# Optimization experiments

Measured on AMD Instinct MI355X. Metric: run time of the kernel, lower is better.

## Reference

```python
import jax, jax.numpy as jnp
import numpy as np

L = 4        # number of GCN layers
B = 1024     # batch of brain graphs
R = 116      # ROIs (AAL atlas)
EPS = 1e-5   # BatchNorm eps


def setup_inputs() -> dict:
    key = jax.random.key(0)
    ks = jax.random.split(key, 20)
    def rn(k, shape, scale=0.1):
        return jax.random.normal(k, shape, dtype=jnp.float32) * scale
    return {
        "X": jax.random.normal(ks[0], (B, R, 3), dtype=jnp.float32),
        "Z": jax.random.normal(ks[1], (B, R, R), dtype=jnp.float32),
        "aw1": rn(ks[2], (L, 3, 3)), "ab1": rn(ks[3], (L, 3)),
        "aw2": rn(ks[4], (L, R, R)), "ab2": rn(ks[5], (L, R)),
        "nw": rn(ks[6], (L, 3, 3)), "nb": rn(ks[7], (L, 3)),
        "ew": rn(ks[8], (L, R, R)), "eb": rn(ks[9], (L, R)),
        "gn_g": jnp.ones((L, R), jnp.float32), "gn_b": jnp.zeros((L, R), jnp.float32),
        "ge_g": jnp.ones((L, R), jnp.float32), "ge_b": jnp.zeros((L, R), jnp.float32),
        "dn_w": rn(ks[10], (L + 1, 3)), "dn_b": rn(ks[11], (L + 1,)),
        "dn_g": jnp.ones((L + 1,), jnp.float32), "dn_beta": jnp.zeros((L + 1,), jnp.float32),
        "de_w": rn(ks[12], (L + 1, 78)), "de_b": rn(ks[13], (L + 1,)),
        "de_g": jnp.ones((L + 1,), jnp.float32), "de_beta": jnp.zeros((L + 1,), jnp.float32),
        "cw1": rn(ks[14], (1024, R * 4 * (L + 1)), 0.02), "cb1": jnp.zeros((1024,), jnp.float32),
        "cw2": rn(ks[15], (2, 1024), 0.02), "cb2": jnp.zeros((2,), jnp.float32),
    }


def _bn3(x, g, b):
    # BatchNorm1d(C) in training mode on (N, C, L): stats over (N, L) per channel
    m = x.mean(axis=(0, 2), keepdims=True)
    v = x.var(axis=(0, 2), keepdims=True)
    return (x - m) * jax.lax.rsqrt(v + EPS) * g[None, :, None] + b[None, :, None]


def _down_node(X, w, b, g, beta):
    # ConvDownSample(3): Conv1d(1,1,3) on (B*R,1,3) -> scalar per row, ReLU, BatchNorm1d(1)
    f = jax.nn.relu(X.reshape(-1, 3) @ w + b)                 # (B*R,)
    h = (f - f.mean()) * jax.lax.rsqrt(f.var() + EPS) * g + beta
    return h.reshape(X.shape[0], -1)                          # (B, R)


def _down_edge(Z, w, b, g, beta):
    # ConvDownSample(116): Conv1d(1,1,78,stride=39,pad=39) -> 3 outputs per row
    x = Z.reshape(-1, R)
    xp = jnp.pad(x, ((0, 0), (39, 39)))                       # (B*R, 194)
    win = jnp.stack([xp[:, 39 * t: 39 * t + 78] for t in range(3)], axis=1)  # (B*R,3,78)
    f = jax.nn.relu(win @ w + b)                              # (B*R, 3)
    h = (f - f.mean()) * jax.lax.rsqrt(f.var() + EPS) * g + beta
    return h.reshape(Z.shape[0], -1)                          # (B, 3R)


def reference(X, Z, aw1, ab1, aw2, ab2, nw, nb, ew, eb, gn_g, gn_b, ge_g, ge_b,
              dn_w, dn_b, dn_g, dn_beta, de_w, de_b, de_g, de_beta,
              cw1, cb1, cw2, cb2):
    xx = [_down_node(X, dn_w[0], dn_b[0], dn_g[0], dn_beta[0])]
    zz = [_down_edge(Z, de_w[0], de_b[0], de_g[0], de_beta[0])]
    for i in range(L):
        # Attention: K = conv1(X^T) (1x1 conv == matmul), Q = K^T, scores = Q@K
        K = jnp.einsum('oc,bnc->bon', aw1[i], X) + ab1[i][None, :, None]   # (B,3,R)
        att = jax.nn.softmax(jnp.einsum('bcn,bcm->bnm', K, K), axis=-1)    # (B,R,R)
        V = jnp.einsum('oc,bmc->bom', aw2[i], Z) + ab2[i][None, :, None]   # (B,R,R)
        A = jnp.einsum('bnk,bkm->bmn', att, V)                             # bmm + permute
        # Edge update
        Z1 = jnp.einsum('bnm,bmc->bnc', A, Z) @ ew[i].T + eb[i]
        Z = jax.nn.relu(_bn3(Z1, ge_g[i], ge_b[i])) + Z
        zz.append(_down_edge(Z, de_w[i + 1], de_b[i + 1], de_g[i + 1], de_beta[i + 1]))
        # Node update
        X1 = jnp.einsum('bnm,bmc->bnc', A, X) @ nw[i].T + nb[i]
        X = jax.nn.relu(_bn3(X1, gn_g[i], gn_b[i])) + X
        xx.append(_down_node(X, dn_w[i + 1], dn_b[i + 1], dn_g[i + 1], dn_beta[i + 1]))
    XZ = jnp.concatenate(xx + zz, axis=1)                     # (B, 116*4*(L+1))
    h = jax.nn.relu(XZ @ cw1.T + cb1)                         # dropout is identity (eval)
    return h @ cw2.T + cb2                                    # (B, 2)
```

## Files before the change

### kernel.cpp

```cpp
#include <hip/hip_runtime.h>
#if __has_include(<hip/hip_bf16.h>)
#include <hip/hip_bf16.h>
#define HAVE_HIP_BF16 1
#endif

#define R 116
#define BATCH 1024
#define NL 4
#define RR2 13456
#define EPSF 1e-5f
#define NZ_ELEM (BATCH * RR2)
#define NX_ELEM (BATCH * R * 3)
#define LS 136
#define XZS 2336
#define NSH 8
#define STL 464
#define NCH 1682

typedef unsigned short ushort_t;
typedef __attribute__((ext_vector_type(8))) short bf16x8;
typedef __attribute__((ext_vector_type(4))) float f32x4;

__device__ __forceinline__ float bf2f(unsigned short u){
  union { unsigned int i; float f; } v; v.i = ((unsigned int)u) << 16; return v.f;
}
__device__ __forceinline__ unsigned short f2bf(float f){
#ifdef HAVE_HIP_BF16
  union { __hip_bfloat16 h; unsigned short u; } cv;
  cv.h = __float2bfloat16(f);
  return cv.u;
#else
  union { float ff; unsigned int i; } v; v.ff = f;
  return (unsigned short)((v.i + 0x7fffu + ((v.i >> 16) & 1u)) >> 16);
#endif
}
__device__ __forceinline__ float u2f_lo(unsigned w){
  union { unsigned i; float f; } v; v.i = w << 16; return v.f;
}
__device__ __forceinline__ float u2f_hi(unsigned w){
  union { unsigned i; float f; } v; v.i = w & 0xffff0000u; return v.f;
}
__device__ __forceinline__ float wsum(float v){
  #pragma unroll
  for (int o = 32; o > 0; o >>= 1) v += __shfl_xor(v, o, 64);
  return v;
}
__device__ __forceinline__ float wmaxr(float v){
  #pragma unroll
  for (int o = 32; o > 0; o >>= 1) v = fmaxf(v, __shfl_xor(v, o, 64));
  return v;
}
__device__ __forceinline__ bf16x8 ldg_z8(const ushort_t* p){
  union { uint2 u2[2]; bf16x8 v; } c;
  c.u2[0] = *(const uint2*)p;
  c.u2[1] = *(const uint2*)(p + 4);
  return c.v;
}

__global__ void k_init(const float4* __restrict__ Zin, uint4* __restrict__ Zc8,
                       const float* __restrict__ Xin, float* __restrict__ Xc,
                       float* __restrict__ st, unsigned* __restrict__ xzw,
                       unsigned* __restrict__ z1g,
                       const float* __restrict__ aw2, const float* __restrict__ ew,
                       ushort_t* __restrict__ aw2p, ushort_t* __restrict__ ewp,
                       const float* __restrict__ cw1, ushort_t* __restrict__ cw1p,
                       const float* __restrict__ cb2, float* __restrict__ out)
{
  int idx = blockIdx.x * 256 + threadIdx.x;
  int stride = gridDim.x * 256;
  for (int i = idx; i < NZ_ELEM/8; i += stride){
    float4 a = Zin[2*i], b = Zin[2*i+1];
    uint4 w;
    w.x = (unsigned)f2bf(a.x) | ((unsigned)f2bf(a.y) << 16);
    w.y = (unsigned)f2bf(a.z) | ((unsigned)f2bf(a.w) << 16);
    w.z = (unsigned)f2bf(b.x) | ((unsigned)f2bf(b.y) << 16);
    w.w = (unsigned)f2bf(b.z) | ((unsigned)f2bf(b.w) << 16);
    Zc8[i] = w;
  }
  for (int i = idx; i < 1024 * XZS; i += stride){
    int n = i / XZS, k = i - n * XZS;
    cw1p[i] = (k < 2320) ? f2bf(cw1[n*2320 + k]) : (ushort_t)0;
  }
  for (int i = idx; i < 4*128*128; i += stride){
    int l = i >> 14, rem = i & 16383, row = rem >> 7, col = rem & 127;
    ushort_t v = 0, w = 0;
    if (row < R && col < R){
      v = f2bf(aw2[l*RR2 + col*R + row]);
      w = f2bf(ew [l*RR2 + row*R + col]);
    }
    aw2p[i] = v;
    ewp [i] = w;
  }
  for (int i = idx; i < NX_ELEM; i += stride) Xc[i] = Xin[i];
  for (int i = idx; i < 15008; i += stride) st[i] = 0.f;
  for (int i = idx; i < BATCH*XZS/2; i += stride) xzw[i] = 0u;
  for (int i = idx; i < 704; i += stride) z1g[i] = 0u;
  for (int i = idx; i < 1024; i += stride){ out[2*i] = cb2[0]; out[2*i+1] = cb2[1]; }
}

__launch_bounds__(1024, 8)
__global__ void k_fused(float* __restrict__ Xc, ushort_t* __restrict__ Zc,
                        ushort_t* __restrict__ Z1, float* __restrict__ X1,
                        const float* __restrict__ aw1, const float* __restrict__ ab1,
                        const ushort_t* __restrict__ aw2p, const float* __restrict__ ab2,
                        const float* __restrict__ nw,  const float* __restrict__ nb,
                        const ushort_t* __restrict__ ewp,  const float* __restrict__ eb,
                        float* __restrict__ zsumS, float* __restrict__ zsqS,
                        float* __restrict__ xsumS, float* __restrict__ xsqS,
                        const float* __restrict__ geg, const float* __restrict__ geb,
                        const float* __restrict__ gng, const float* __restrict__ gnb,
                        const float* __restrict__ dnw, const float* __restrict__ dnb,
                        const float* __restrict__ dew, const float* __restrict__ deb,
                        ushort_t* __restrict__ XZ,
                        float* __restrict__ dnS, float* __restrict__ deS,
                        int layer, int with_attn)
{
  __shared__ __align__(16) ushort_t bA[128*LS];
  __shared__ __align__(16) ushort_t bB[128*LS];
  __shared__ float Ksm[3*R];
  __shared__ float ssm[R];
  __shared__ float xp[R*12];
  __shared__ float zps[128*2];
  __shared__ float zpq[128*2];
  __shared__ float wsm[78];
  __shared__ float xsred[3], xqred[3];
  __shared__ float zds[8], zqs[8];

  float* zcoA = xp;
  float* zcoC = xp + 116;
  float* xcoA = xp + 232;
  float* xcoC = xp + 348;
  ushort_t* bBlin = bB;

  const int b    = blockIdx.x;
  const int tid  = threadIdx.x;
  const int lane = tid & 63;
  const int wave = tid >> 6;
  const int qm   = lane & 15;
  const int quad = lane >> 4;
  const int tr   = wave & 7;
  const int tc0  = (wave >> 3) * 4;
  const int t_snap = layer;
  const int sh   = b & (NSH-1);

  ushort_t* Zb = Zc + (size_t)b * RR2;
  const ushort_t* Z1b = Z1 + (size_t)b * RR2;
  const float* ab2l = ab2 + layer * R;
  const float* ebl  = eb  + layer * R;
  const float* nwl  = nw  + layer * 9;
  const float* nbl  = nb  + layer * 3;
  const ushort_t* aw2l = aw2p + layer * 16384;
  const ushort_t* ewl  = ewp  + layer * 16384;

  const f32x4 vzero = {0.f, 0.f, 0.f, 0.f};

  if (tid < R){
    float a = 0.f, c = 0.f;
    if (layer > 0){
      const int pl = layer - 1;
      float ms = 0.f, qs = 0.f;
      #pragma unroll
      for (int s2 = 0; s2 < NSH; s2++){
        ms += zsumS[s2*STL + pl*R + tid];
        qs += zsqS [s2*STL + pl*R + tid];
      }
      const float cnt = (float)(BATCH * R);
      float m  = ms / cnt;
      float va = fmaxf(qs / cnt - m*m, 0.f);
      float rs = rsqrtf(va + EPSF);
      a = rs * geg[pl*R + tid];
      c = geb[pl*R + tid] - m * a;
    }
    zcoA[tid] = a; zcoC[tid] = c;
  } else if (tid >= 128 && tid < 128 + R){
    const int r = tid - 128;
    float a = 0.f, c = 0.f;
    if (layer > 0){
      const int pl = layer - 1;
      float ms = 0.f, qs = 0.f;
      #pragma unroll
      for (int s2 = 0; s2 < NSH; s2++){
        ms += xsumS[s2*STL + pl*R + r];
        qs += xsqS [s2*STL + pl*R + r];
      }
      const float cnt = (float)(BATCH * 3);
      float m  = ms / cnt;
      float va = fmaxf(qs / cnt - m*m, 0.f);
      float rs = rsqrtf(va + EPSF);
      a = rs * gng[pl*R + r];
      c = gnb[pl*R + r] - m * a;
    }
    xcoA[r] = a; xcoC[r] = c;
  } else if (tid >= 256 && tid < 256 + 78){
    wsm[tid - 256] = dew[t_snap*78 + (tid - 256)];
  }
  __syncthreads();

  {
    const int ch0 = tid;
    const int ch1 = tid + 1024;
    const bool hasB = (ch1 < NCH);
    const int e0A = ch0 << 3;
    const int e0B = ch1 << 3;
    uint4 zcA = *(const uint4*)(Zb + e0A);
    uint4 zcB; if (hasB) zcB = *(const uint4*)(Zb + e0B);
    if (layer > 0){
      uint4 z1A = *(const uint4*)(Z1b + e0A);
      uint4 z1B; if (hasB) z1B = *(const uint4*)(Z1b + e0B);
      #pragma unroll
      for (int half = 0; half < 2; half++){
        if (half == 1 && !hasB) break;
        const int e0 = half ? e0B : e0A;
        const uint4 zc4 = half ? zcB : zcA;
        const uint4 z14 = half ? z1B : z1A;
        const int r0 = e0 / 116;
        const int c0 = e0 - r0*116;
        float aA = zcoA[r0], cA = zcoC[r0];
        float aB = aA, cB = cA;
        if (c0 == 112){ aB = zcoA[r0+1]; cB = zcoC[r0+1]; }
        const unsigned zw[4]  = {zc4.x, zc4.y, zc4.z, zc4.w};
        const unsigned z1w[4] = {z14.x, z14.y, z14.z, z14.w};
        unsigned ow[4];
        #pragma unroll
        for (int h = 0; h < 4; h++){
          float aa = (h < 2) ? aA : aB;
          float cc = (h < 2) ? cA : cB;
          float vL = fmaxf(u2f_lo(z1w[h])*aa + cc, 0.f) + u2f_lo(zw[h]);
          float vH = fmaxf(u2f_hi(z1w[h])*aa + cc, 0.f) + u2f_hi(zw[h]);
          ow[h] = (unsigned)f2bf(vL) | ((unsigned)f2bf(vH) << 16);
        }
        uint4 o; o.x = ow[0]; o.y = ow[1]; o.z = ow[2]; o.w = ow[3];
        if (with_attn) *(uint4*)(Zb + e0) = o;
        *(uint4*)&bBlin[e0] = o;
      }
    } else {
      *(uint4*)&bBlin[e0A] = zcA;
      if (hasB) *(uint4*)&bBlin[e0B] = zcB;
    }
  }
  {
    float fv = 0.f;
    if (tid >= 658 && tid < 658 + R){
      const int u = tid - 658;
      float* xcr = Xc + ((size_t)b*R + u)*3;
      float v0, v1, v2;
      if (layer > 0){
        float a = xcoA[u], c = xcoC[u];
        const float* x1r = X1 + ((size_t)b*R + u)*3;
        v0 = fmaxf(x1r[0]*a + c, 0.f) + xcr[0];
        v1 = fmaxf(x1r[1]*a + c, 0.f) + xcr[1];
        v2 = fmaxf(x1r[2]*a + c, 0.f) + xcr[2];
        if (with_attn){ xcr[0] = v0; xcr[1] = v1; xcr[2] = v2; }
      } else {
        v0 = xcr[0]; v1 = xcr[1]; v2 = xcr[2];
      }
      if (with_attn){
        const float* aw1l = aw1 + layer * 9;
        const float* ab1l = ab1 + layer * 3;
        #pragma unroll
        for (int o = 0; o < 3; o++)
          Ksm[o*R + u] = ab1l[o] + aw1l[o*3+0]*v0 + aw1l[o*3+1]*v1 + aw1l[o*3+2]*v2;
      }
      float f = fmaxf(dnw[t_snap*3+0]*v0 + dnw[t_snap*3+1]*v1 + dnw[t_snap*3+2]*v2 + dnb[t_snap], 0.f);
      XZ[(size_t)b*XZS + t_snap*R + u] = f2bf(f);
      fv = f;
    }
    if (wave >= 10 && wave <= 12){
      float s = wsum(fv), q = wsum(fv*fv);
      if (lane == 0){ xsred[wave - 10] = s; xqred[wave - 10] = q; }
    }
  }
  if (tid >= 774){
    for (int i = tid - 774; i < 12*LS; i += 250) bA[116*LS + i] = 0;
    for (int i = tid - 774; i < 116*20; i += 250){
      int r = i/20, c = 116 + (i - r*20);
      bA[r*LS + c] = 0;
    }
  }
  __syncthreads();

  if (wave < 10){
    if (tid == 0){
      atomicAdd(&dnS[sh*10 + t_snap*2+0], xsred[0] + xsred[1] + xsred[2]);
      atomicAdd(&dnS[sh*10 + t_snap*2+1], xqred[0] + xqred[1] + xqred[2]);
    }
    if (with_attn){
      for (int n = wave; n < R; n += 10){
        float k0 = Ksm[n], k1 = Ksm[R+n], k2 = Ksm[2*R+n];
        int m0 = lane, m1 = lane + 64;
        float a0 = k0*Ksm[m0] + k1*Ksm[R+m0] + k2*Ksm[2*R+m0];
        float a1 = (m1 < R) ? (k0*Ksm[m1] + k1*Ksm[R+m1] + k2*Ksm[2*R+m1]) : -1e30f;
        float mx = wmaxr(fmaxf(a0, a1));
        float e0 = __expf(a0 - mx);
        float e1 = (m1 < R) ? __expf(a1 - mx) : 0.f;
        float sm = wsum(e0 + e1);
        float sab = wsum(e0 * ab2l[m0] + ((m1 < R) ? e1 * ab2l[m1] : 0.f));
        float inv = 1.f / sm;
        bA[n*LS + m0] = f2bf(e0 * inv);
        if (m1 < R) bA[n*LS + m1] = f2bf(e1 * inv);
        if (lane == 0) ssm[n] = sab * inv;
      }
    }
  } else {
    const int u = tid - 640;
    float f = 0.f;
    if (u < 348){
      int r = u / 3, w = u - 3*r;
      int jlo = (w == 0) ? 39 : 0;
      int jhi = (w == 2) ? 77 : 78;
      int off = (w - 1) * 39;
      const ushort_t* vr = &bBlin[r*116];
      float acc = 0.f;
      for (int j = jlo; j < jhi; j++) acc += wsm[j] * bf2f(vr[j + off]);
      f = fmaxf(acc + deb[t_snap], 0.f);
      XZ[(size_t)b*XZS + 5*R + t_snap*3*R + r*3 + w] = f2bf(f);
    }
    float s = wsum(f), q = wsum(f*f);
    if (lane == 0){ zds[wave - 10] = s; zqs[wave - 10] = q; }
  }
  __syncthreads();

  if (tid == 0){
    float ss = 0.f, qq = 0.f;
    #pragma unroll
    for (int k = 0; k < 6; k++){ ss += zds[k]; qq += zqs[k]; }
    atomicAdd(&deS[sh*10 + t_snap*2+0], ss);
    atomicAdd(&deS[sh*10 + t_snap*2+1], qq);
  }
  if (!with_attn) return;

  {
    f32x4 acc[4];
    #pragma unroll
    for (int t = 0; t < 4; t++) acc[t] = vzero;
    for (int kk = 0; kk < 128; kk += 32){
      bf16x8 a = *(const bf16x8*)(aw2l + (tr*16 + qm)*128 + kk + quad*8);
      #pragma unroll
      for (int t = 0; t < 4; t++){
        bf16x8 bf = *(const bf16x8*)&bA[((tc0 + t)*16 + qm)*LS + kk + quad*8];
        acc[t] = __builtin_amdgcn_mfma_f32_16x16x32_bf16(a, bf, acc[t], 0, 0, 0);
      }
    }
    const int r0 = tr*16 + quad*4;
    #pragma unroll
    for (int t = 0; t < 4; t++){
      int nn = (tc0 + t)*16 + qm;
      uint2 w;
      w.x = (unsigned)f2bf(acc[t][0]) | ((unsigned)f2bf(acc[t][1]) << 16);
      w.y = (unsigned)f2bf(acc[t][2]) | ((unsigned)f2bf(acc[t][3]) << 16);
      *(uint2*)&bB[nn*LS + r0] = w;
    }
  }
  __syncthreads();

  {
    f32x4 acc[4];
    #pragma unroll
    for (int t = 0; t < 4; t++) acc[t] = vzero;
    for (int kk = 0; kk < 128; kk += 32){
      bf16x8 a = *(const bf16x8*)&bB[(tr*16 + qm)*LS + kk + quad*8];
      #pragma unroll
      for (int t = 0; t < 4; t++){
        int nn = (tc0 + t)*16 + qm;
        bf16x8 bf = ldg_z8(Zb + nn*R + kk + quad*8);
        acc[t] = __builtin_amdgcn_mfma_f32_16x16x32_bf16(a, bf, acc[t], 0, 0, 0);
      }
    }
    const int r0 = tr*16 + quad*4;
    float s0 = 0.f, s1 = 0.f, s2 = 0.f, s3 = 0.f;
    if (r0 < R){ s0 = ssm[r0]; s1 = ssm[r0+1]; s2 = ssm[r0+2]; s3 = ssm[r0+3]; }
    #pragma unroll
    for (int t = 0; t < 4; t++){
      int nn = (tc0 + t)*16 + qm;
      uint2 w;
      w.x = (unsigned)f2bf(acc[t][0] + s0) | ((unsigned)f2bf(acc[t][1] + s1) << 16);
      w.y = (unsigned)f2bf(acc[t][2] + s2) | ((unsigned)f2bf(acc[t][3] + s3) << 16);
      *(uint2*)&bA[nn*LS + r0] = w;
    }
  }
  __syncthreads();

  {
    f32x4 acc[4];
    #pragma unroll
    for (int t = 0; t < 4; t++) acc[t] = vzero;
    for (int kk = 0; kk < 128; kk += 32){
      bf16x8 a = ldg_z8(Zb + (tr*16 + qm)*R + kk + quad*8);
      #pragma unroll
      for (int t = 0; t < 4; t++){
        bf16x8 bf = *(const bf16x8*)(ewl + ((tc0 + t)*16 + qm)*128 + kk + quad*8);
        acc[t] = __builtin_amdgcn_mfma_f32_16x16x32_bf16(a, bf, acc[t], 0, 0, 0);
      }
    }
    const int r0 = tr*16 + quad*4;
    #pragma unroll
    for (int t = 0; t < 4; t++){
      int nn = (tc0 + t)*16 + qm;
      uint2 w;
      w.x = (unsigned)f2bf(acc[t][0]) | ((unsigned)f2bf(acc[t][1]) << 16);
      w.y = (unsigned)f2bf(acc[t][2]) | ((unsigned)f2bf(acc[t][3]) << 16);
      *(uint2*)&bB[nn*LS + r0] = w;
    }
  }
  __syncthreads();

  {
    f32x4 acc[4];
    #pragma unroll
    for (int t = 0; t < 4; t++) acc[t] = vzero;
    for (int kk = 0; kk < 128; kk += 32){
      bf16x8 a = *(const bf16x8*)&bA[(tr*16 + qm)*LS + kk + quad*8];
      #pragma unroll
      for (int t = 0; t < 4; t++){
        bf16x8 bf = *(const bf16x8*)&bB[((tc0 + t)*16 + qm)*LS + kk + quad*8];
        acc[t] = __builtin_amdgcn_mfma_f32_16x16x32_bf16(a, bf, acc[t], 0, 0, 0);
      }
    }
    float ssv[4] = {0.f,0.f,0.f,0.f}, sqv[4] = {0.f,0.f,0.f,0.f};
    #pragma unroll
    for (int t = 0; t < 4; t++){
      int col = (tc0 + t)*16 + qm;
      float bias = (col < R) ? ebl[col] : 0.f;
      #pragma unroll
      for (int rg = 0; rg < 4; rg++){
        int row = tr*16 + quad*4 + rg;
        float v = (col < R) ? (acc[t][rg] + bias) : 0.f;
        if (col < R && row < R)
          Z1[(size_t)b*RR2 + row*R + col] = f2bf(v);
        ssv[rg] += v; sqv[rg] += v*v;
      }
    }
    #pragma unroll
    for (int off = 1; off < 16; off <<= 1){
      #pragma unroll
      for (int rg = 0; rg < 4; rg++){
        ssv[rg] += __shfl_xor(ssv[rg], off, 64);
        sqv[rg] += __shfl_xor(sqv[rg], off, 64);
      }
    }
    if (qm == 0){
      int half = wave >> 3;
      #pragma unroll
      for (int rg = 0; rg < 4; rg++){
        int row = tr*16 + quad*4 + rg;
        zps[row*2 + half] = ssv[rg];
        zpq[row*2 + half] = sqv[rg];
      }
    }
  }

  const float* Xb = Xc + (size_t)b * R * 3;
  if (tid < R*4){
    int n = tid >> 2, part = tid & 3;
    const ushort_t* rowp = &bA[n*LS];
    float t0 = 0.f, t1 = 0.f, t2 = 0.f;
    for (int mb = part*4; mb < 116; mb += 16){
      uint2 w = *(const uint2*)(rowp + mb);
      float p0 = u2f_lo(w.x), p1 = u2f_hi(w.x), p2 = u2f_lo(w.y), p3 = u2f_hi(w.y);
      const float* x4 = Xb + mb*3;
      t0 = fmaf(p0, x4[0], fmaf(p1, x4[3], fmaf(p2, x4[6], fmaf(p3, x4[9],  t0))));
      t1 = fmaf(p0, x4[1], fmaf(p1, x4[4], fmaf(p2, x4[7], fmaf(p3, x4[10], t1))));
      t2 = fmaf(p0, x4[2], fmaf(p1, x4[5], fmaf(p2, x4[8], fmaf(p3, x4[11], t2))));
    }
    xp[tid*3+0] = t0; xp[tid*3+1] = t1; xp[tid*3+2] = t2;
  }
  __syncthreads();
  if (tid < R){
    float c0 = xp[tid*12+0] + xp[tid*12+3] + xp[tid*12+6] + xp[tid*12+9];
    float c1 = xp[tid*12+1] + xp[tid*12+4] + xp[tid*12+7] + xp[tid*12+10];
    float c2 = xp[tid*12+2] + xp[tid*12+5] + xp[tid*12+8] + xp[tid*12+11];
    float s = 0.f, q = 0.f;
    #pragma unroll
    for (int e = 0; e < 3; e++){
      float v = nbl[e] + c0*nwl[e*3+0] + c1*nwl[e*3+1] + c2*nwl[e*3+2];
      X1[((size_t)b*R + tid)*3 + e] = v;
      s += v; q += v*v;
    }
    atomicAdd(&xsumS[sh*STL + layer*R + tid], s);
    atomicAdd(&xsqS [sh*STL + layer*R + tid], q);
    atomicAdd(&zsumS[sh*STL + layer*R + tid], zps[tid*2] + zps[tid*2+1]);
    atomicAdd(&zsqS [sh*STL + layer*R + tid], zpq[tid*2] + zpq[tid*2+1]);
  }
}

__global__ void k_applyAll(const float* __restrict__ dnS, const float* __restrict__ deS,
                           const float* __restrict__ dng, const float* __restrict__ dnbe,
                           const float* __restrict__ deg, const float* __restrict__ debe,
                           ushort_t* __restrict__ XZ)
{
  int idx = blockIdx.x * 256 + threadIdx.x;
  int bi = idx / R, r = idx - bi*R;
  const float cn = (float)(BATCH * R);
  const float ce = (float)(BATCH * R * 3);
  #pragma unroll
  for (int t = 0; t < 5; t++){
    float dns = 0.f, dnq = 0.f, des = 0.f, deq = 0.f;
    #pragma unroll
    for (int s2 = 0; s2 < NSH; s2++){
      dns += dnS[s2*10 + t*2+0]; dnq += dnS[s2*10 + t*2+1];
      des += deS[s2*10 + t*2+0]; deq += deS[s2*10 + t*2+1];
    }
    float mn = dns / cn;
    float vn = fmaxf(dnq / cn - mn*mn, 0.f);
    size_t sn = (size_t)bi*XZS + t*R + r;
    float hn = (bf2f(XZ[sn]) - mn) * rsqrtf(vn + EPSF) * dng[t] + dnbe[t];
    XZ[sn] = f2bf(hn);
    float me = des / ce;
    float ve = fmaxf(deq / ce - me*me, 0.f);
    float rse = rsqrtf(ve + EPSF);
    size_t se = (size_t)bi*XZS + 5*R + t*3*R + r*3;
    #pragma unroll
    for (int p = 0; p < 3; p++){
      float he = (bf2f(XZ[se+p]) - me) * rse * deg[t] + debe[t];
      XZ[se+p] = f2bf(he);
    }
  }
}

__launch_bounds__(256)
__global__ void k_fc(const ushort_t* __restrict__ XZ, const ushort_t* __restrict__ cw1p,
                     const float* __restrict__ cb1, const float* __restrict__ cw2,
                     float* __restrict__ out){
  const int tid  = threadIdx.x;
  const int lane = tid & 63;
  const int wave = tid >> 6;
  const int qm   = lane & 15;
  const int quad = lane >> 4;
  const int m0   = blockIdx.x * 64 + wave * 16;
  const int n0   = blockIdx.y * 64;

  const f32x4 vzero = {0.f, 0.f, 0.f, 0.f};
  f32x4 acc[4];
  #pragma unroll
  for (int t = 0; t < 4; t++) acc[t] = vzero;

  const ushort_t* arow = XZ + (size_t)(m0 + qm) * XZS;
  for (int kk = 0; kk < XZS; kk += 32){
    bf16x8 a = *(const bf16x8*)(arow + kk + quad*8);
    #pragma unroll
    for (int t = 0; t < 4; t++){
      const ushort_t* brow = cw1p + (size_t)(n0 + t*16 + qm) * XZS;
      bf16x8 bf = *(const bf16x8*)(brow + kk + quad*8);
      acc[t] = __builtin_amdgcn_mfma_f32_16x16x32_bf16(a, bf, acc[t], 0, 0, 0);
    }
  }
  #pragma unroll
  for (int rg = 0; rg < 4; rg++){
    float p0 = 0.f, p1 = 0.f;
    #pragma unroll
    for (int t = 0; t < 4; t++){
      int n = n0 + t*16 + qm;
      float h = fmaxf(acc[t][rg] + cb1[n], 0.f);
      p0 = fmaf(h, cw2[n], p0);
      p1 = fmaf(h, cw2[1024 + n], p1);
    }
    #pragma unroll
    for (int o = 1; o < 16; o <<= 1){
      p0 += __shfl_xor(p0, o, 64);
      p1 += __shfl_xor(p1, o, 64);
    }
    if (qm == 0){
      int m = m0 + quad*4 + rg;
      atomicAdd(&out[m*2 + 0], p0);
      atomicAdd(&out[m*2 + 1], p1);
    }
  }
}

extern "C" void kernel_launch(void* const* d_in, const int* in_sizes, int n_in,
                              void* d_out, int out_size, void* d_ws, size_t ws_size,
                              hipStream_t stream)
{
  const float* Xin  = (const float*)d_in[0];
  const float* Zin  = (const float*)d_in[1];
  const float* aw1  = (const float*)d_in[2];
  const float* ab1  = (const float*)d_in[3];
  const float* aw2  = (const float*)d_in[4];
  const float* ab2  = (const float*)d_in[5];
  const float* nw   = (const float*)d_in[6];
  const float* nb   = (const float*)d_in[7];
  const float* ew   = (const float*)d_in[8];
  const float* eb   = (const float*)d_in[9];
  const float* gng  = (const float*)d_in[10];
  const float* gnb  = (const float*)d_in[11];
  const float* geg  = (const float*)d_in[12];
  const float* geb  = (const float*)d_in[13];
  const float* dnw  = (const float*)d_in[14];
  const float* dnb  = (const float*)d_in[15];
  const float* dng  = (const float*)d_in[16];
  const float* dnbe = (const float*)d_in[17];
  const float* dew  = (const float*)d_in[18];
  const float* deb  = (const float*)d_in[19];
  const float* deg  = (const float*)d_in[20];
  const float* debe = (const float*)d_in[21];
  const float* cw1  = (const float*)d_in[22];
  const float* cb1  = (const float*)d_in[23];
  const float* cw2  = (const float*)d_in[24];
  const float* cb2  = (const float*)d_in[25];

  ushort_t* Zc = (ushort_t*)d_ws;
  ushort_t* Z1 = Zc + NZ_ELEM;
  float*    Xc = (float*)(Z1 + NZ_ELEM);
  float*    X1 = Xc + NX_ELEM;
  ushort_t* XZ = (ushort_t*)(X1 + NX_ELEM);
  float*    st = (float*)(XZ + BATCH*XZS);
  float* zsumS = st;
  float* zsqS  = st + 3712;
  float* xsumS = st + 7424;
  float* xsqS  = st + 11136;
  float* dnS   = st + 14848;
  float* deS   = st + 14928;
  ushort_t* aw2p = (ushort_t*)(st + 15008);
  ushort_t* ewp  = aw2p + 4*16384;
  ushort_t* cw1p = ewp + 4*16384;

  float* outp = (float*)d_out;

  k_init<<<4096, 256, 0, stream>>>((const float4*)Zin, (uint4*)Zc, Xin, Xc,
                                   st, (unsigned*)XZ, (unsigned*)Z1,
                                   aw2, ew, aw2p, ewp, cw1, cw1p, cb2, outp);

  for (int i = 0; i < NL; i++){
    k_fused<<<BATCH, 1024, 0, stream>>>(Xc, Zc, Z1, X1, aw1, ab1, aw2p, ab2,
                                        nw, nb, ewp, eb, zsumS, zsqS, xsumS, xsqS,
                                        geg, geb, gng, gnb, dnw, dnb, dew, deb,
                                        XZ, dnS, deS, i, 1);
  }
  k_fused<<<BATCH, 1024, 0, stream>>>(Xc, Zc, Z1, X1, aw1, ab1, aw2p, ab2,
                                      nw, nb, ewp, eb, zsumS, zsqS, xsumS, xsqS,
                                      geg, geb, gng, gnb, dnw, dnb, dew, deb,
                                      XZ, dnS, deS, NL, 0);

  k_applyAll<<<464, 256, 0, stream>>>(dnS, deS, dng, dnbe, deg, debe, XZ);

  k_fc<<<dim3(16, 16), 256, 0, stream>>>(XZ, cw1p, cb1, cw2, outp);
}
```

Before: 650.9 us.

## Pad resident Z rows to 120 elements for aligned 16-byte loads

Stores the bf16 Z state with a row pitch of 120 instead of 116, so each 8-element chunk lies inside one row and is 16-byte aligned. MFMA operand loads of Z become single 128-bit loads instead of pairs of 64-bit loads, and the residual-update path no longer needs cross-row coefficient handling. The cost is about 3% more Z memory traffic, Z1 reads that now use four 32-bit loads per chunk because Z1 keeps its unpadded layout, and a per-element index divide in the init kernel.

```diff
diff --git a/kernel.cpp b/kernel.cpp
--- a/kernel.cpp
+++ b/kernel.cpp
@@ -5,17 +5,20 @@
 #endif
 
 #define R 116
+#define RP 120
+#define GZ 13920
 #define BATCH 1024
 #define NL 4
 #define RR2 13456
 #define EPSF 1e-5f
+#define NZP_ELEM (BATCH * GZ)
 #define NZ_ELEM (BATCH * RR2)
 #define NX_ELEM (BATCH * R * 3)
 #define LS 136
 #define XZS 2336
 #define NSH 8
 #define STL 464
-#define NCH 1682
+#define NCHP 1740
 
 typedef unsigned short ushort_t;
 typedef __attribute__((ext_vector_type(8))) short bf16x8;
@@ -50,14 +53,8 @@
   for (int o = 32; o > 0; o >>= 1) v = fmaxf(v, __shfl_xor(v, o, 64));
   return v;
 }
-__device__ __forceinline__ bf16x8 ldg_z8(const ushort_t* p){
-  union { uint2 u2[2]; bf16x8 v; } c;
-  c.u2[0] = *(const uint2*)p;
-  c.u2[1] = *(const uint2*)(p + 4);
-  return c.v;
-}
-
-__global__ void k_init(const float4* __restrict__ Zin, uint4* __restrict__ Zc8,
+
+__global__ void k_init(const float* __restrict__ Zin, ushort_t* __restrict__ Zcp,
                        const float* __restrict__ Xin, float* __restrict__ Xc,
                        float* __restrict__ st, unsigned* __restrict__ xzw,
                        unsigned* __restrict__ z1g,
@@ -68,14 +65,21 @@
 {
   int idx = blockIdx.x * 256 + threadIdx.x;
   int stride = gridDim.x * 256;
-  for (int i = idx; i < NZ_ELEM/8; i += stride){
-    float4 a = Zin[2*i], b = Zin[2*i+1];
+  for (int i = idx; i < BATCH * NCHP; i += stride){
+    int g = i / NCHP, ch = i - g * NCHP;
+    int e0 = ch << 3, r = e0 / RP, c0 = e0 - r * RP;
+    const float* zi = Zin + (size_t)g * RR2 + r * R + c0;
+    float4 f0 = *(const float4*)zi;
     uint4 w;
-    w.x = (unsigned)f2bf(a.x) | ((unsigned)f2bf(a.y) << 16);
-    w.y = (unsigned)f2bf(a.z) | ((unsigned)f2bf(a.w) << 16);
-    w.z = (unsigned)f2bf(b.x) | ((unsigned)f2bf(b.y) << 16);
-    w.w = (unsigned)f2bf(b.z) | ((unsigned)f2bf(b.w) << 16);
-    Zc8[i] = w;
+    w.x = (unsigned)f2bf(f0.x) | ((unsigned)f2bf(f0.y) << 16);
+    w.y = (unsigned)f2bf(f0.z) | ((unsigned)f2bf(f0.w) << 16);
+    if (c0 == 112){ w.z = 0u; w.w = 0u; }
+    else {
+      float4 f1 = *(const float4*)(zi + 4);
+      w.z = (unsigned)f2bf(f1.x) | ((unsigned)f2bf(f1.y) << 16);
+      w.w = (unsigned)f2bf(f1.z) | ((unsigned)f2bf(f1.w) << 16);
+    }
+    *(uint4*)(Zcp + (size_t)g * GZ + e0) = w;
   }
   for (int i = idx; i < 1024 * XZS; i += stride){
     int n = i / XZS, k = i - n * XZS;
@@ -94,7 +98,7 @@
   for (int i = idx; i < NX_ELEM; i += stride) Xc[i] = Xin[i];
   for (int i = idx; i < 15008; i += stride) st[i] = 0.f;
   for (int i = idx; i < BATCH*XZS/2; i += stride) xzw[i] = 0u;
-  for (int i = idx; i < 704; i += stride) z1g[i] = 0u;
+  for (int i = idx; i < 736; i += stride) z1g[i] = 0u;
   for (int i = idx; i < 1024; i += stride){ out[2*i] = cb2[0]; out[2*i+1] = cb2[1]; }
 }
 
@@ -143,7 +147,7 @@
   const int t_snap = layer;
   const int sh   = b & (NSH-1);
 
-  ushort_t* Zb = Zc + (size_t)b * RR2;
+  ushort_t* Zb = Zc + (size_t)b * GZ;
   const ushort_t* Z1b = Z1 + (size_t)b * RR2;
   const float* ab2l = ab2 + layer * R;
   const float* ebl  = eb  + layer * R;
@@ -199,36 +203,41 @@
   {
     const int ch0 = tid;
     const int ch1 = tid + 1024;
-    const bool hasB = (ch1 < NCH);
+    const bool hasB = (ch1 < NCHP);
     const int e0A = ch0 << 3;
     const int e0B = ch1 << 3;
     uint4 zcA = *(const uint4*)(Zb + e0A);
     uint4 zcB; if (hasB) zcB = *(const uint4*)(Zb + e0B);
     if (layer > 0){
-      uint4 z1A = *(const uint4*)(Z1b + e0A);
-      uint4 z1B; if (hasB) z1B = *(const uint4*)(Z1b + e0B);
+      const int rA = e0A / RP, cA0 = e0A - rA*RP;
+      const int rB = hasB ? (e0B / RP) : 0, cB0 = hasB ? (e0B - rB*RP) : 0;
+      const ushort_t* z1pA = Z1b + rA*R + cA0;
+      const ushort_t* z1pB = Z1b + rB*R + cB0;
+      unsigned z1A[4], z1B[4];
+      #pragma unroll
+      for (int i = 0; i < 4; i++) z1A[i] = *(const unsigned*)(z1pA + 2*i);
+      if (hasB){
+        #pragma unroll
+        for (int i = 0; i < 4; i++) z1B[i] = *(const unsigned*)(z1pB + 2*i);
+      }
       #pragma unroll
       for (int half = 0; half < 2; half++){
         if (half == 1 && !hasB) break;
         const int e0 = half ? e0B : e0A;
+        const int r  = half ? rB  : rA;
+        const int c0 = half ? cB0 : cA0;
         const uint4 zc4 = half ? zcB : zcA;
-        const uint4 z14 = half ? z1B : z1A;
-        const int r0 = e0 / 116;
-        const int c0 = e0 - r0*116;
-        float aA = zcoA[r0], cA = zcoC[r0];
-        float aB = aA, cB = cA;
-        if (c0 == 112){ aB = zcoA[r0+1]; cB = zcoC[r0+1]; }
-        const unsigned zw[4]  = {zc4.x, zc4.y, zc4.z, zc4.w};
-        const unsigned z1w[4] = {z14.x, z14.y, z14.z, z14.w};
+        const unsigned* z1w = half ? z1B : z1A;
+        const float aa = zcoA[r], cc = zcoC[r];
+        const unsigned zw[4] = {zc4.x, zc4.y, zc4.z, zc4.w};
         unsigned ow[4];
         #pragma unroll
         for (int h = 0; h < 4; h++){
-          float aa = (h < 2) ? aA : aB;
-          float cc = (h < 2) ? cA : cB;
           float vL = fmaxf(u2f_lo(z1w[h])*aa + cc, 0.f) + u2f_lo(zw[h]);
           float vH = fmaxf(u2f_hi(z1w[h])*aa + cc, 0.f) + u2f_hi(zw[h]);
           ow[h] = (unsigned)f2bf(vL) | ((unsigned)f2bf(vH) << 16);
         }
+        if (c0 == 112){ ow[2] = 0u; ow[3] = 0u; }
         uint4 o; o.x = ow[0]; o.y = ow[1]; o.z = ow[2]; o.w = ow[3];
         if (with_attn) *(uint4*)(Zb + e0) = o;
         *(uint4*)&bBlin[e0] = o;
@@ -309,7 +318,7 @@
       int jlo = (w == 0) ? 39 : 0;
       int jhi = (w == 2) ? 77 : 78;
       int off = (w - 1) * 39;
-      const ushort_t* vr = &bBlin[r*116];
+      const ushort_t* vr = &bBlin[r*RP];
       float acc = 0.f;
       for (int j = jlo; j < jhi; j++) acc += wsm[j] * bf2f(vr[j + off]);
       f = fmaxf(acc + deb[t_snap], 0.f);
@@ -362,7 +371,7 @@
       #pragma unroll
       for (int t = 0; t < 4; t++){
         int nn = (tc0 + t)*16 + qm;
-        bf16x8 bf = ldg_z8(Zb + nn*R + kk + quad*8);
+        bf16x8 bf = *(const bf16x8*)(Zb + nn*RP + kk + quad*8);
         acc[t] = __builtin_amdgcn_mfma_f32_16x16x32_bf16(a, bf, acc[t], 0, 0, 0);
       }
     }
@@ -385,7 +394,7 @@
     #pragma unroll
     for (int t = 0; t < 4; t++) acc[t] = vzero;
     for (int kk = 0; kk < 128; kk += 32){
-      bf16x8 a = ldg_z8(Zb + (tr*16 + qm)*R + kk + quad*8);
+      bf16x8 a = *(const bf16x8*)(Zb + (tr*16 + qm)*RP + kk + quad*8);
       #pragma unroll
       for (int t = 0; t < 4; t++){
         bf16x8 bf = *(const bf16x8*)(ewl + ((tc0 + t)*16 + qm)*128 + kk + quad*8);
@@ -599,7 +608,7 @@
   const float* cb2  = (const float*)d_in[25];
 
   ushort_t* Zc = (ushort_t*)d_ws;
-  ushort_t* Z1 = Zc + NZ_ELEM;
+  ushort_t* Z1 = Zc + NZP_ELEM;
   float*    Xc = (float*)(Z1 + NZ_ELEM);
   float*    X1 = Xc + NX_ELEM;
   ushort_t* XZ = (ushort_t*)(X1 + NX_ELEM);
@@ -616,7 +625,7 @@
 
   float* outp = (float*)d_out;
 
-  k_init<<<4096, 256, 0, stream>>>((const float4*)Zin, (uint4*)Zc, Xin, Xc,
+  k_init<<<4096, 256, 0, stream>>>(Zin, Zc, Xin, Xc,
                                    st, (unsigned*)XZ, (unsigned*)Z1,
                                    aw2, ew, aw2p, ewp, cw1, cw1p, cb2, outp);
 
```

After: 653.3 us. About the same (+0.4%).
